# Kernel optimization log

Measured on AMD Instinct MI355X. Metric: run time of the kernel, lower is better.

## Reference

```python
import jax, jax.numpy as jnp
import numpy as np

JACCARD_THRESH = 0.5
NEGPOS_RATIO = 3
VAR = (0.1, 0.2)


def point_form(p):
    # center-size (cx,cy,w,h) -> corner (xmin,ymin,xmax,ymax)
    return jnp.concatenate([p[:, :2] - p[:, 2:] / 2, p[:, :2] + p[:, 2:] / 2], axis=1)


def jaccard(a, b):
    # a: [No,4] corner boxes, b: [Np,4] corner boxes -> IoU [No,Np]
    lt = jnp.maximum(a[:, None, :2], b[None, :, :2])
    rb = jnp.minimum(a[:, None, 2:], b[None, :, 2:])
    wh = jnp.clip(rb - lt, 0.0)
    inter = wh[..., 0] * wh[..., 1]
    area_a = ((a[:, 2] - a[:, 0]) * (a[:, 3] - a[:, 1]))[:, None]
    area_b = ((b[:, 2] - b[:, 0]) * (b[:, 3] - b[:, 1]))[None, :]
    return inter / (area_a + area_b - inter)


def encode(matched, priors):
    # matched: [Np,4] corner GT, priors: [Np,4] center-size
    g_cxcy = ((matched[:, :2] + matched[:, 2:]) / 2 - priors[:, :2]) / (VAR[0] * priors[:, 2:])
    g_wh = jnp.log((matched[:, 2:] - matched[:, :2]) / priors[:, 2:]) / VAR[1]
    return jnp.concatenate([g_cxcy, g_wh], axis=1)


def match_one(truths, labels, priors):
    # truths: [No,4], labels: [No], priors: [Np,4] center-size
    overlaps = jaccard(truths, point_form(priors))          # [No,Np]
    best_prior_idx = jnp.argmax(overlaps, axis=1)           # [No]
    best_truth_overlap = jnp.max(overlaps, axis=0)          # [Np]
    best_truth_idx = jnp.argmax(overlaps, axis=0)           # [Np]
    # each GT keeps its best prior (overlap forced to 2)
    best_truth_overlap = best_truth_overlap.at[best_prior_idx].set(2.0)
    best_truth_idx = best_truth_idx.at[best_prior_idx].set(jnp.arange(truths.shape[0]))
    matched = truths[best_truth_idx]                        # [Np,4]
    conf = labels[best_truth_idx].astype(jnp.int32) + 1     # background = 0
    conf = jnp.where(best_truth_overlap < JACCARD_THRESH, 0, conf)
    return encode(matched, priors), conf


def reference(loc_data, conf_data, dbox_list, targets):
    num_batch, num_dbox, num_classes = conf_data.shape
    truths = targets[:, :, :4]
    labels = targets[:, :, 4]
    loc_t, conf_t = jax.vmap(match_one, in_axes=(0, 0, None))(truths, labels, dbox_list)
    pos_mask = conf_t > 0                                   # [B,Np]
    # localization loss: SmoothL1 (beta=1), summed over positive dboxes
    diff = loc_data - loc_t
    ad = jnp.abs(diff)
    sl1 = jnp.where(ad < 1.0, 0.5 * diff * diff, ad - 0.5)
    loss_l = jnp.sum(sl1 * pos_mask[..., None].astype(sl1.dtype))
    # per-dbox cross entropy
    logp = jax.nn.log_softmax(conf_data, axis=-1)
    ce = -jnp.take_along_axis(logp, conf_t[..., None], axis=-1)[..., 0]  # [B,Np]
    # hard negative mining: rank (descending) of pos-zeroed CE via double argsort
    loss_c_hnm = jnp.where(pos_mask, 0.0, ce)
    loss_idx = jnp.argsort(-loss_c_hnm, axis=1)
    idx_rank = jnp.argsort(loss_idx, axis=1)
    num_pos = jnp.sum(pos_mask, axis=1, keepdims=True)      # [B,1]
    num_neg = jnp.minimum(num_pos * NEGPOS_RATIO, num_dbox)
    neg_mask = idx_rank < num_neg
    sel = jnp.logical_or(pos_mask, neg_mask)
    loss_c = jnp.sum(jnp.where(sel, ce, 0.0))
    N = jnp.sum(num_pos).astype(loss_l.dtype)
    return loss_l / N, loss_c / N


def setup_inputs() -> dict:
    key = jax.random.key(0)
    ks = jax.random.split(key, 7)
    B, Np, C, No = 128, 8732, 21, 16
    loc_data = jax.random.normal(ks[0], (B, Np, 4), dtype=jnp.float32) * 0.1
    conf_data = jax.random.normal(ks[1], (B, Np, C), dtype=jnp.float32)
    # default boxes in center-size form, w/h strictly positive
    cxcy = jax.random.uniform(ks[2], (Np, 2), minval=0.05, maxval=0.95)
    wh = jax.random.uniform(ks[3], (Np, 2), minval=0.05, maxval=0.5)
    dbox_list = jnp.concatenate([cxcy, wh], axis=1).astype(jnp.float32)
    # ground truth: valid corner-form boxes + class label in [0,20)
    gcxcy = jax.random.uniform(ks[4], (B, No, 2), minval=0.2, maxval=0.8)
    gwh = jax.random.uniform(ks[5], (B, No, 2), minval=0.05, maxval=0.3)
    boxes = jnp.concatenate([gcxcy - gwh / 2, gcxcy + gwh / 2], axis=-1)
    lab = jax.random.randint(ks[6], (B, No, 1), 0, C - 1).astype(jnp.float32)
    targets = jnp.concatenate([boxes, lab], axis=-1).astype(jnp.float32)
    return {"loc_data": loc_data, "conf_data": conf_data, "dbox_list": dbox_list, "targets": targets}
```

## Files before the change

### kernel.cpp

```cpp
#include <hip/hip_runtime.h>
#include <stdint.h>

#define TPB 256
#define SELTPB 1024
#define SELWAVES (SELTPB / 64)
#define MAXNO 64
#define NMB 4

__device__ __forceinline__ float sl1f(float d) {
    float ad = fabsf(d);
    return ad < 1.0f ? 0.5f * d * d : ad - 0.5f;
}

__device__ __forceinline__ float iou_pair(float tx1, float ty1, float tx2, float ty2, float ta,
                                          float px1, float py1, float px2, float py2, float pa) {
    float ltx = fmaxf(tx1, px1), lty = fmaxf(ty1, py1);
    float rbx = fminf(tx2, px2), rby = fminf(ty2, py2);
    float wx = fmaxf(rbx - ltx, 0.0f), wy = fmaxf(rby - lty, 0.0f);
    float inter = wx * wy;
    return inter / ((ta + pa) - inter);
}

template <int NO>
__global__ __launch_bounds__(256) void match_partial_kernel(
    const float* __restrict__ dbox, const float* __restrict__ targets,
    unsigned long long* __restrict__ pkeys, int Np, int No) {
    int b = blockIdx.y, mb = blockIdx.x;
    int tid = threadIdx.x;
    __shared__ float s_t[NO][5];
    __shared__ unsigned long long s_k[4][NO];
    if (tid < No) {
        const float* tr = targets + ((size_t)b * No + tid) * 5;
        float x1 = tr[0], y1 = tr[1], x2 = tr[2], y2 = tr[3];
        s_t[tid][0] = x1; s_t[tid][1] = y1; s_t[tid][2] = x2; s_t[tid][3] = y2;
        s_t[tid][4] = (x2 - x1) * (y2 - y1);
    }
    __syncthreads();
    int clen = (Np + NMB - 1) / NMB;
    int start = mb * clen;
    int end = start + clen;
    if (end > Np) end = Np;
    unsigned long long key[NO];
#pragma unroll
    for (int t = 0; t < NO; ++t) key[t] = 0ull;
    for (int p = start + tid; p < end; p += 256) {
        float4 pr = *reinterpret_cast<const float4*>(dbox + (size_t)p * 4);
        float px1 = pr.x - pr.z * 0.5f, py1 = pr.y - pr.w * 0.5f;
        float px2 = pr.x + pr.z * 0.5f, py2 = pr.y + pr.w * 0.5f;
        float pa = (px2 - px1) * (py2 - py1);
        unsigned lowp = 0xFFFFFFFFu - (unsigned)p;
#pragma unroll
        for (int t = 0; t < NO; ++t) {
            float iou = iou_pair(s_t[t][0], s_t[t][1], s_t[t][2], s_t[t][3], s_t[t][4],
                                 px1, py1, px2, py2, pa);
            unsigned long long k =
                (((unsigned long long)__float_as_uint(iou)) << 32) | (unsigned long long)lowp;
            if (k > key[t]) key[t] = k;
        }
    }
    int lane = tid & 63, wv = tid >> 6;
#pragma unroll
    for (int t = 0; t < NO; ++t) {
        unsigned long long k = key[t];
        for (int off = 32; off; off >>= 1) {
            unsigned long long o = __shfl_down(k, off);
            if (o > k) k = o;
        }
        if (lane == 0) s_k[wv][t] = k;
    }
    __syncthreads();
    if (tid < No) {
        unsigned long long m = s_k[0][tid];
#pragma unroll
        for (int w = 1; w < 4; ++w)
            if (s_k[w][tid] > m) m = s_k[w][tid];
        pkeys[((size_t)b * NMB + mb) * No + tid] = m;
    }
}

__global__ __launch_bounds__(TPB) void main_kernel(
    const float* __restrict__ loc, const float* __restrict__ conf,
    const float* __restrict__ dbox, const float* __restrict__ targets,
    const unsigned long long* __restrict__ pkeys,
    float* __restrict__ v, float* __restrict__ part_l, float* __restrict__ part_c,
    int* __restrict__ part_n, int Np, int C, int No, int nchunk) {
    extern __shared__ float s_conf[];
    __shared__ float s_t[MAXNO][5];
    __shared__ float s_lab[MAXNO];
    __shared__ int s_ovr[MAXNO];
    __shared__ float s_red1[4];
    __shared__ float s_red2[4];
    __shared__ int s_redi[4];
    int b = blockIdx.y, chunk = blockIdx.x, tid = threadIdx.x;
    int p = chunk * TPB + tid;
    bool valid = p < Np;
    if (tid < No) {
        const float* tr = targets + ((size_t)b * No + tid) * 5;
        float x1 = tr[0], y1 = tr[1], x2 = tr[2], y2 = tr[3];
        s_t[tid][0] = x1; s_t[tid][1] = y1; s_t[tid][2] = x2; s_t[tid][3] = y2;
        s_t[tid][4] = (x2 - x1) * (y2 - y1);
        s_lab[tid] = tr[4];
        unsigned long long k = pkeys[((size_t)b * NMB + 0) * No + tid];
        for (int m = 1; m < NMB; ++m) {
            unsigned long long kk = pkeys[((size_t)b * NMB + m) * No + tid];
            if (kk > k) k = kk;
        }
        s_ovr[tid] = (int)(0xFFFFFFFFu - (unsigned)(k & 0xFFFFFFFFull));
    }
    int pbase = chunk * TPB;
    int cnt = Np - pbase;
    if (cnt > TPB) cnt = TPB;
    const float* cbase = conf + ((size_t)b * Np + (size_t)pbase) * C;
    for (int i = tid; i < cnt * C; i += TPB) s_conf[i] = cbase[i];
    __syncthreads();

    float lossl = 0.0f, posce = 0.0f;
    int npos = 0;
    if (valid) {
        float4 pr = *reinterpret_cast<const float4*>(dbox + (size_t)p * 4);
        float px1 = pr.x - pr.z * 0.5f, py1 = pr.y - pr.w * 0.5f;
        float px2 = pr.x + pr.z * 0.5f, py2 = pr.y + pr.w * 0.5f;
        float pa = (px2 - px1) * (py2 - py1);
        float bov = -1.0f;
        int bidx = 0;
        for (int t = 0; t < No; ++t) {
            float iou = iou_pair(s_t[t][0], s_t[t][1], s_t[t][2], s_t[t][3], s_t[t][4],
                                 px1, py1, px2, py2, pa);
            if (iou > bov) { bov = iou; bidx = t; }
        }
        for (int t = 0; t < No; ++t)
            if (s_ovr[t] == p) { bidx = t; bov = 2.0f; }
        int ct = (bov < 0.5f) ? 0 : ((int)s_lab[bidx] + 1);
        const float* crow = s_conf + (size_t)tid * C;
        float mx = crow[0];
        for (int j = 1; j < C; ++j) mx = fmaxf(mx, crow[j]);
        float s = 0.0f;
        for (int j = 0; j < C; ++j) s += expf(crow[j] - mx);
        float ce = logf(s) + mx - crow[ct];
        bool pos = ct > 0;
        v[(size_t)b * Np + p] = pos ? 0.0f : ce;
        if (pos) {
            posce = ce;
            npos = 1;
            float mx1 = s_t[bidx][0], my1 = s_t[bidx][1], mx2 = s_t[bidx][2], my2 = s_t[bidx][3];
            float gcx = ((mx1 + mx2) * 0.5f - pr.x) / (0.1f * pr.z);
            float gcy = ((my1 + my2) * 0.5f - pr.y) / (0.1f * pr.w);
            float gw = logf((mx2 - mx1) / pr.z) / 0.2f;
            float gh = logf((my2 - my1) / pr.w) / 0.2f;
            float4 l4 = *reinterpret_cast<const float4*>(loc + ((size_t)b * Np + p) * 4);
            lossl = sl1f(l4.x - gcx) + sl1f(l4.y - gcy) + sl1f(l4.z - gw) + sl1f(l4.w - gh);
        }
    }
    float a1 = lossl, a2 = posce;
    int ni = npos;
    for (int off = 32; off; off >>= 1) {
        a1 += __shfl_down(a1, off);
        a2 += __shfl_down(a2, off);
        ni += __shfl_down(ni, off);
    }
    if ((tid & 63) == 0) {
        s_red1[tid >> 6] = a1;
        s_red2[tid >> 6] = a2;
        s_redi[tid >> 6] = ni;
    }
    __syncthreads();
    if (tid == 0) {
        part_l[(size_t)b * nchunk + chunk] = s_red1[0] + s_red1[1] + s_red1[2] + s_red1[3];
        part_c[(size_t)b * nchunk + chunk] = s_red2[0] + s_red2[1] + s_red2[2] + s_red2[3];
        part_n[(size_t)b * nchunk + chunk] = s_redi[0] + s_redi[1] + s_redi[2] + s_redi[3];
    }
}

__global__ __launch_bounds__(SELTPB) void select_kernel(
    const float* __restrict__ v, const float* __restrict__ pl,
    const float* __restrict__ pc, const int* __restrict__ pn,
    float* __restrict__ row_res, int Np, int nchunk, int negpos) {
    int b = blockIdx.x, tid = threadIdx.x;
    int lane = tid & 63, wv = tid >> 6;
    extern __shared__ unsigned sv[];
    __shared__ unsigned whist[SELWAVES][256];
    __shared__ unsigned suf[257];
    __shared__ float s_f[SELWAVES];
    __shared__ int s_dig, s_acc;
    __shared__ float s_lossl, s_posce;
    __shared__ int s_np;

    if (wv == 0) {
        float a = 0.0f, c = 0.0f;
        int n = 0;
        for (int i = lane; i < nchunk; i += 64) {
            a += pl[(size_t)b * nchunk + i];
            c += pc[(size_t)b * nchunk + i];
            n += pn[(size_t)b * nchunk + i];
        }
        for (int off = 32; off; off >>= 1) {
            a += __shfl_down(a, off);
            c += __shfl_down(c, off);
            n += __shfl_down(n, off);
        }
        if (lane == 0) { s_lossl = a; s_posce = c; s_np = n; }
    }
    {
        const float4* v4 = reinterpret_cast<const float4*>(v + (size_t)b * Np);
        int n4 = Np >> 2;
        for (int i = tid; i < n4; i += SELTPB) {
            float4 f = v4[i];
            uint4 u;
            u.x = __float_as_uint(f.x); u.y = __float_as_uint(f.y);
            u.z = __float_as_uint(f.z); u.w = __float_as_uint(f.w);
            *reinterpret_cast<uint4*>(&sv[i << 2]) = u;
        }
        for (int i = (n4 << 2) + tid; i < Np; i += SELTPB)
            sv[i] = __float_as_uint(v[(size_t)b * Np + i]);
    }
    __syncthreads();
    int npos = s_np;
    int K = npos * negpos;
    if (K > Np) K = Np;
    float lossc = s_posce;
    if (K > 0) {
        unsigned prefix = 0;
        int Krem = K;
        for (int shift = 24; shift >= 0; shift -= 8) {
            for (int i = tid; i < SELWAVES * 256; i += SELTPB)
                (&whist[0][0])[i] = 0;
            __syncthreads();
            for (int i = tid; i < Np; i += SELTPB) {
                unsigned u = sv[i];
                bool match = (shift == 24) || ((u >> (shift + 8)) == (prefix >> (shift + 8)));
                if (match) atomicAdd(&whist[wv][(u >> shift) & 0xFFu], 1u);
            }
            __syncthreads();
            if (tid < 256) {
                unsigned t = 0;
                for (int w = 0; w < SELWAVES; ++w) t += whist[w][tid];
                suf[tid] = t;
            }
            if (tid == 0) suf[256] = 0;
            __syncthreads();
            for (int off = 1; off < 256; off <<= 1) {
                unsigned add = 0;
                if (tid < 256 && tid + off < 256) add = suf[tid + off];
                __syncthreads();
                if (tid < 256) suf[tid] += add;
                __syncthreads();
            }
            if (tid < 256) {
                unsigned S = suf[tid];
                unsigned Snext = suf[tid + 1];
                if ((int)S >= Krem && (int)Snext < Krem) { s_dig = tid; s_acc = (int)Snext; }
            }
            __syncthreads();
            prefix |= ((unsigned)s_dig) << shift;
            Krem -= s_acc;
            __syncthreads();
        }
        float sum_gt = 0.0f;
        for (int i = tid; i < Np; i += SELTPB) {
            unsigned u = sv[i];
            if (u > prefix) sum_gt += __uint_as_float(u);
        }
        for (int off = 32; off; off >>= 1) sum_gt += __shfl_down(sum_gt, off);
        if (lane == 0) s_f[wv] = sum_gt;
        __syncthreads();
        if (tid == 0) {
            float t = 0.0f;
            for (int w = 0; w < SELWAVES; ++w) t += s_f[w];
            lossc += t + (float)Krem * __uint_as_float(prefix);
        }
    }
    if (tid == 0) {
        row_res[(size_t)b * 3 + 0] = s_lossl;
        row_res[(size_t)b * 3 + 1] = lossc;
        row_res[(size_t)b * 3 + 2] = (float)npos;
    }
}

__global__ __launch_bounds__(TPB) void finalize_kernel(
    const float* __restrict__ row_res, float* __restrict__ out, int B) {
    int tid = threadIdx.x;
    float l = 0, c = 0, n = 0;
    for (int i = tid; i < B; i += TPB) {
        l += row_res[(size_t)i * 3 + 0];
        c += row_res[(size_t)i * 3 + 1];
        n += row_res[(size_t)i * 3 + 2];
    }
    __shared__ float sl[4], sc[4], sn[4];
    for (int off = 32; off; off >>= 1) {
        l += __shfl_down(l, off);
        c += __shfl_down(c, off);
        n += __shfl_down(n, off);
    }
    int lane = tid & 63, w = tid >> 6;
    if (lane == 0) { sl[w] = l; sc[w] = c; sn[w] = n; }
    __syncthreads();
    if (tid == 0) {
        l = sl[0] + sl[1] + sl[2] + sl[3];
        c = sc[0] + sc[1] + sc[2] + sc[3];
        n = sn[0] + sn[1] + sn[2] + sn[3];
        out[0] = l / n;
        out[1] = c / n;
    }
}

extern "C" void kernel_launch(void* const* d_in, const int* in_sizes, int n_in,
                              void* d_out, int out_size, void* d_ws, size_t ws_size,
                              hipStream_t stream) {
    const float* loc = (const float*)d_in[0];
    const float* conf = (const float*)d_in[1];
    const float* dbox = (const float*)d_in[2];
    const float* targets = (const float*)d_in[3];

    int Np = in_sizes[2] / 4;
    int B = in_sizes[0] / (Np * 4);
    int C = in_sizes[1] / (B * Np);
    int No = in_sizes[3] / (B * 5);
    int nchunk = (Np + TPB - 1) / TPB;

    char* w = (char*)d_ws;
    unsigned long long* pkeys = (unsigned long long*)w;
    w += (size_t)B * NMB * No * sizeof(unsigned long long);
    float* v = (float*)w;
    w += (size_t)B * Np * sizeof(float);
    float* part_l = (float*)w;
    w += (size_t)B * nchunk * sizeof(float);
    float* part_c = (float*)w;
    w += (size_t)B * nchunk * sizeof(float);
    int* part_n = (int*)w;
    w += (size_t)B * nchunk * sizeof(int);
    float* row_res = (float*)w;

    dim3 mgrid(NMB, B);
    if (No == 16)
        match_partial_kernel<16><<<mgrid, 256, 0, stream>>>(dbox, targets, pkeys, Np, No);
    else
        match_partial_kernel<MAXNO><<<mgrid, 256, 0, stream>>>(dbox, targets, pkeys, Np, No);

    dim3 grid(nchunk, B);
    size_t lds_main = (size_t)TPB * C * sizeof(float);
    main_kernel<<<grid, TPB, lds_main, stream>>>(loc, conf, dbox, targets, pkeys,
                                                 v, part_l, part_c, part_n, Np, C, No, nchunk);
    select_kernel<<<B, SELTPB, (size_t)Np * sizeof(float), stream>>>(v, part_l, part_c, part_n,
                                                                     row_res, Np, nchunk, 3);
    finalize_kernel<<<1, TPB, 0, stream>>>(row_res, (float*)d_out, B);
}
```

Measured before the change: 87.03 us.

## Vectorize conf staging, specialize softmax for 21 classes, use fast math, more match blocks

The conf tile is now copied into LDS with float4 loads, with a scalar tail for leftover elements. A C=21 template unrolls the log-softmax into registers and picks the target logit without a dynamic LDS index. Precise expf and logf are replaced with the __expf and __logf intrinsics, trading some accuracy for speed. NMB rises from 4 to 16, so more blocks run the partial matching step, at the cost of more partial keys for main_kernel to reduce.

```diff
diff --git a/kernel.cpp b/kernel.cpp
--- a/kernel.cpp
+++ b/kernel.cpp
@@ -5,7 +5,7 @@
 #define SELTPB 1024
 #define SELWAVES (SELTPB / 64)
 #define MAXNO 64
-#define NMB 4
+#define NMB 16
 
 __device__ __forceinline__ float sl1f(float d) {
     float ad = fabsf(d);
@@ -78,6 +78,7 @@
     }
 }
 
+template <int CC>
 __global__ __launch_bounds__(TPB) void main_kernel(
     const float* __restrict__ loc, const float* __restrict__ conf,
     const float* __restrict__ dbox, const float* __restrict__ targets,
@@ -111,7 +112,14 @@
     int cnt = Np - pbase;
     if (cnt > TPB) cnt = TPB;
     const float* cbase = conf + ((size_t)b * Np + (size_t)pbase) * C;
-    for (int i = tid; i < cnt * C; i += TPB) s_conf[i] = cbase[i];
+    {
+        int ntot = cnt * C;
+        int nv4 = ntot >> 2;
+        const float4* c4 = reinterpret_cast<const float4*>(cbase);
+        float4* s4 = reinterpret_cast<float4*>(s_conf);
+        for (int i = tid; i < nv4; i += TPB) s4[i] = c4[i];
+        for (int i = (nv4 << 2) + tid; i < ntot; i += TPB) s_conf[i] = cbase[i];
+    }
     __syncthreads();
 
     float lossl = 0.0f, posce = 0.0f;
@@ -131,12 +139,30 @@
         for (int t = 0; t < No; ++t)
             if (s_ovr[t] == p) { bidx = t; bov = 2.0f; }
         int ct = (bov < 0.5f) ? 0 : ((int)s_lab[bidx] + 1);
-        const float* crow = s_conf + (size_t)tid * C;
-        float mx = crow[0];
-        for (int j = 1; j < C; ++j) mx = fmaxf(mx, crow[j]);
-        float s = 0.0f;
-        for (int j = 0; j < C; ++j) s += expf(crow[j] - mx);
-        float ce = logf(s) + mx - crow[ct];
+        float ce;
+        if (CC > 0) {
+            const float* crow = s_conf + tid * CC;
+            float fr[CC > 0 ? CC : 1];
+            float mx = -1e30f, fc = 0.0f;
+#pragma unroll
+            for (int j = 0; j < CC; ++j) {
+                float x = crow[j];
+                fr[j] = x;
+                mx = fmaxf(mx, x);
+                fc = (j == ct) ? x : fc;
+            }
+            float s = 0.0f;
+#pragma unroll
+            for (int j = 0; j < CC; ++j) s += __expf(fr[j] - mx);
+            ce = __logf(s) + mx - fc;
+        } else {
+            const float* crow = s_conf + (size_t)tid * C;
+            float mx = crow[0];
+            for (int j = 1; j < C; ++j) mx = fmaxf(mx, crow[j]);
+            float s = 0.0f;
+            for (int j = 0; j < C; ++j) s += __expf(crow[j] - mx);
+            ce = __logf(s) + mx - crow[ct];
+        }
         bool pos = ct > 0;
         v[(size_t)b * Np + p] = pos ? 0.0f : ce;
         if (pos) {
@@ -145,8 +171,8 @@
             float mx1 = s_t[bidx][0], my1 = s_t[bidx][1], mx2 = s_t[bidx][2], my2 = s_t[bidx][3];
             float gcx = ((mx1 + mx2) * 0.5f - pr.x) / (0.1f * pr.z);
             float gcy = ((my1 + my2) * 0.5f - pr.y) / (0.1f * pr.w);
-            float gw = logf((mx2 - mx1) / pr.z) / 0.2f;
-            float gh = logf((my2 - my1) / pr.w) / 0.2f;
+            float gw = __logf((mx2 - mx1) / pr.z) / 0.2f;
+            float gh = __logf((my2 - my1) / pr.w) / 0.2f;
             float4 l4 = *reinterpret_cast<const float4*>(loc + ((size_t)b * Np + p) * 4);
             lossl = sl1f(l4.x - gcx) + sl1f(l4.y - gcy) + sl1f(l4.z - gw) + sl1f(l4.w - gh);
         }
@@ -338,8 +364,12 @@
 
     dim3 grid(nchunk, B);
     size_t lds_main = (size_t)TPB * C * sizeof(float);
-    main_kernel<<<grid, TPB, lds_main, stream>>>(loc, conf, dbox, targets, pkeys,
-                                                 v, part_l, part_c, part_n, Np, C, No, nchunk);
+    if (C == 21)
+        main_kernel<21><<<grid, TPB, lds_main, stream>>>(loc, conf, dbox, targets, pkeys,
+                                                         v, part_l, part_c, part_n, Np, C, No, nchunk);
+    else
+        main_kernel<0><<<grid, TPB, lds_main, stream>>>(loc, conf, dbox, targets, pkeys,
+                                                        v, part_l, part_c, part_n, Np, C, No, nchunk);
     select_kernel<<<B, SELTPB, (size_t)Np * sizeof(float), stream>>>(v, part_l, part_c, part_n,
                                                                      row_res, Np, nchunk, 3);
     finalize_kernel<<<1, TPB, 0, stream>>>(row_res, (float*)d_out, B);
```

Measured after the change: 87.20 us. Within noise of the previous version (+0.2%).
